# Performance work log

Measured on AMD Instinct MI355X. Metric: run time of the kernel, lower is better.

## Reference

```python
import jax, jax.numpy as jnp
import numpy as np

N = 50000      # nodes
E = 800000     # edges (avg degree 16)
IN_DIM = 128
H = 64         # hidden (GINSmall default)
C = 2          # n_classes
G = 64         # number of graphs in batch


def setup_inputs() -> dict:
    key = jax.random.key(0)
    ks = jax.random.split(key, 16)
    s = 0.05
    inp = {
        "x": jax.random.normal(ks[0], (N, IN_DIM), dtype=jnp.float32),
        "edge_index": jax.random.randint(ks[1], (2, E), 0, N, dtype=jnp.int64),
        "batch": jnp.sort(jax.random.randint(ks[2], (N,), 0, G, dtype=jnp.int64)),
        # conv 0 MLP
        "W1_0": jax.random.normal(ks[3], (IN_DIM, H), dtype=jnp.float32) * s,
        "b1_0": jnp.zeros((H,), jnp.float32),
        "W2_0": jax.random.normal(ks[4], (H, H), dtype=jnp.float32) * s,
        "b2_0": jnp.zeros((H,), jnp.float32),
        # conv 1 MLP
        "W1_1": jax.random.normal(ks[5], (H, H), dtype=jnp.float32) * s,
        "b1_1": jnp.zeros((H,), jnp.float32),
        "W2_1": jax.random.normal(ks[6], (H, H), dtype=jnp.float32) * s,
        "b2_1": jnp.zeros((H,), jnp.float32),
        # conv 2 MLP
        "W1_2": jax.random.normal(ks[7], (H, H), dtype=jnp.float32) * s,
        "b1_2": jnp.zeros((H,), jnp.float32),
        "W2_2": jax.random.normal(ks[8], (H, H), dtype=jnp.float32) * s,
        "b2_2": jnp.zeros((H,), jnp.float32),
        # readout
        "Wl": jax.random.normal(ks[9], (H, C), dtype=jnp.float32) * s,
        "bl": jnp.zeros((C,), jnp.float32),
    }
    return inp


def _gin_conv(h, src, dst, W1, b1, W2, b2):
    # GINConv with eps=0: MLP(h_i + sum_{j->i} h_j)
    agg = jax.ops.segment_sum(h[src], dst, num_segments=N)  # [N, d]
    z = h + agg
    return jnp.maximum(z @ W1 + b1, 0.0) @ W2 + b2


def reference(x, edge_index, batch,
              W1_0, b1_0, W2_0, b2_0,
              W1_1, b1_1, W2_1, b2_1,
              W1_2, b1_2, W2_2, b2_2,
              Wl, bl):
    src, dst = edge_index[0], edge_index[1]  # PyG: messages flow src -> dst
    params = [(W1_0, b1_0, W2_0, b2_0),
              (W1_1, b1_1, W2_1, b2_1),
              (W1_2, b1_2, W2_2, b2_2)]
    h = x
    for (W1, b1, W2, b2) in params:
        h = _gin_conv(h, src, dst, W1, b1, W2, b2)
        h = jnp.maximum(h, 0.0)  # ReLU; dropout is identity at inference
    # global mean pool over graph ids
    sums = jax.ops.segment_sum(h, batch, num_segments=G)          # [G, H]
    cnt = jax.ops.segment_sum(jnp.ones((N,), h.dtype), batch, num_segments=G)
    g = sums / jnp.maximum(cnt, 1.0)[:, None]
    out = g @ Wl + bl
    return out, g
```

## Files before the change

kernel.cpp:

```cpp
#include <hip/hip_runtime.h>

typedef unsigned short ushort_t;
typedef __attribute__((ext_vector_type(8))) short short8;
typedef __attribute__((ext_vector_type(4))) float f32x4;

__device__ inline float bflo(unsigned int u) { return __uint_as_float(u << 16); }
__device__ inline float bfhi(unsigned int u) { return __uint_as_float(u & 0xFFFF0000u); }
__device__ inline unsigned short f2bf(float f) {
    unsigned int u = __float_as_uint(f);
    return (unsigned short)((u + 0x7FFFu + ((u >> 16) & 1u)) >> 16);
}
__device__ inline unsigned int pk(float a, float b) {
    return (unsigned int)f2bf(a) | ((unsigned int)f2bf(b) << 16);
}

union U16B { uint4 u; short8 s; };

__global__ __launch_bounds__(256) void hist_rank(const int* __restrict__ dst,
                                                 int* __restrict__ deg,
                                                 int* __restrict__ rank, int E) {
    int e = blockIdx.x * 256 + threadIdx.x;
    if (e < E) rank[e] = atomicAdd(&deg[dst[e]], 1);
}

__global__ __launch_bounds__(256) void scan_reduce(const int* __restrict__ deg,
                                                   int* __restrict__ bsum, int n) {
    __shared__ int sdata[256];
    int base = blockIdx.x * 1024 + threadIdx.x * 4;
    int s = 0;
#pragma unroll
    for (int k = 0; k < 4; k++) { int i = base + k; if (i < n) s += deg[i]; }
    sdata[threadIdx.x] = s;
    __syncthreads();
    for (int off = 128; off > 0; off >>= 1) {
        if (threadIdx.x < off) sdata[threadIdx.x] += sdata[threadIdx.x + off];
        __syncthreads();
    }
    if (threadIdx.x == 0) bsum[blockIdx.x] = sdata[0];
}

__global__ void scan_bsum(int* __restrict__ bsum, int nb, int* __restrict__ rowptr, int n) {
    if (threadIdx.x == 0 && blockIdx.x == 0) {
        int acc = 0;
        for (int i = 0; i < nb; i++) { int v = bsum[i]; bsum[i] = acc; acc += v; }
        rowptr[n] = acc;
    }
}

__global__ __launch_bounds__(256) void scan_final(const int* __restrict__ deg,
                                                  const int* __restrict__ bsum,
                                                  int* __restrict__ rowptr, int n) {
    __shared__ int sdata[256];
    int t = threadIdx.x;
    int base = blockIdx.x * 1024 + t * 4;
    int v[4]; int s = 0;
#pragma unroll
    for (int k = 0; k < 4; k++) { int i = base + k; v[k] = (i < n) ? deg[i] : 0; s += v[k]; }
    sdata[t] = s;
    __syncthreads();
    for (int off = 1; off < 256; off <<= 1) {
        int x = 0;
        if (t >= off) x = sdata[t - off];
        __syncthreads();
        if (t >= off) sdata[t] += x;
        __syncthreads();
    }
    int off = bsum[blockIdx.x] + sdata[t] - s;
#pragma unroll
    for (int k = 0; k < 4; k++) {
        int i = base + k;
        if (i < n) { rowptr[i] = off; off += v[k]; }
    }
}

__global__ __launch_bounds__(256) void fill_range(const int* __restrict__ src,
                                                  const int* __restrict__ dst,
                                                  const int* __restrict__ rank,
                                                  const int* __restrict__ rowptr,
                                                  int* __restrict__ col, int E, int CE) {
    int range = blockIdx.x & 7;
    int sub = blockIdx.x >> 3;
    int e0 = sub * CE;
    int e1 = min(e0 + CE, E);
    for (int e = e0 + threadIdx.x; e < e1; e += 256) {
        int d = dst[e];
        if ((d >> 13) == range) col[rowptr[d] + rank[e]] = src[e];
    }
}

__global__ __launch_bounds__(256) void gemm_y_mfma(const float* __restrict__ x,
                                                   const float* __restrict__ W1,
                                                   ushort_t* __restrict__ Y, int n) {
    __shared__ ushort_t w1f[4][4][64][8];
    __shared__ ushort_t ybuf[64][72];
    for (int i = threadIdx.x; i < 8192; i += 256) {
        int j = i & 7, lane = (i >> 3) & 63, ct = (i >> 9) & 3, ks = (i >> 11) & 3;
        int k = ks * 32 + ((lane >> 4) << 3) + j;
        int c = ct * 16 + (lane & 15);
        w1f[ks][ct][lane][j] = f2bf(W1[k * 64 + c]);
    }
    __syncthreads();
    int w = threadIdx.x >> 6, lane = threadIdx.x & 63;
    int row0 = blockIdx.x * 64;
    int arow = row0 + w * 16 + (lane & 15);
    if (arow >= n) arow = n - 1;
    const float* xr = x + (size_t)arow * 128;
    int k0base = (lane >> 4) << 3;

    f32x4 acc[4] = {{0,0,0,0},{0,0,0,0},{0,0,0,0},{0,0,0,0}};
#pragma unroll
    for (int ks = 0; ks < 4; ks++) {
        int k0 = ks * 32 + k0base;
        float4 aa = *(const float4*)(xr + k0);
        float4 ab = *(const float4*)(xr + k0 + 4);
        U16B af;
        af.u.x = pk(aa.x, aa.y);
        af.u.y = pk(aa.z, aa.w);
        af.u.z = pk(ab.x, ab.y);
        af.u.w = pk(ab.z, ab.w);
#pragma unroll
        for (int ct = 0; ct < 4; ct++) {
            short8 bf = *(const short8*)&w1f[ks][ct][lane][0];
            acc[ct] = __builtin_amdgcn_mfma_f32_16x16x32_bf16(af.s, bf, acc[ct], 0, 0, 0);
        }
    }
#pragma unroll
    for (int ct = 0; ct < 4; ct++)
#pragma unroll
        for (int r = 0; r < 4; r++)
            ybuf[w * 16 + ((lane >> 4) << 2) + r][ct * 16 + (lane & 15)] = f2bf(acc[ct][r]);
    __syncthreads();
    int row = threadIdx.x >> 2, seg = threadIdx.x & 3;
    if (row0 + row < n) {
        const uint4* p = (const uint4*)&ybuf[row][seg * 16];
        uint4 v0 = p[0], v1 = p[1];
        uint4* q = (uint4*)(Y + (size_t)(row0 + row) * 64 + seg * 16);
        q[0] = v0; q[1] = v1;
    }
}

template <int HASNEXT>
__global__ __launch_bounds__(256) void gfuse(const ushort_t* __restrict__ Y,
                                             const int* __restrict__ rowptr,
                                             const int* __restrict__ col,
                                             const float* __restrict__ b1,
                                             const float* __restrict__ W2,
                                             const float* __restrict__ b2,
                                             const float* __restrict__ Wn,
                                             ushort_t* __restrict__ Yn,
                                             const int* __restrict__ batch,
                                             float* __restrict__ sums, int n) {
    __shared__ ushort_t w2f[2][4][64][8];
    __shared__ ushort_t wnf[HASNEXT ? 2 : 1][4][64][8];
    __shared__ ushort_t st[64][72];
    __shared__ float vbuf[HASNEXT ? 1 : 64][65];
    __shared__ float b1s[64], b2s[64];
    for (int i = threadIdx.x; i < 4096; i += 256) {
        int j = i & 7, lane = (i >> 3) & 63, ct = (i >> 9) & 3, ks = (i >> 11) & 1;
        int k = ks * 32 + ((lane >> 4) << 3) + j;
        int c = ct * 16 + (lane & 15);
        w2f[ks][ct][lane][j] = f2bf(W2[k * 64 + c]);
        if (HASNEXT) wnf[ks][ct][lane][j] = f2bf(Wn[k * 64 + c]);
    }
    if (threadIdx.x < 64) { b1s[threadIdx.x] = b1[threadIdx.x]; b2s[threadIdx.x] = b2[threadIdx.x]; }
    __syncthreads();

    int row0 = blockIdx.x * 64;

    {
        int lr = threadIdx.x >> 2;
        int q  = threadIdx.x & 3;
        int gnode = row0 + lr;
        uint4 o0, o1;
        if (gnode < n) {
            const ushort_t* yb = Y + (size_t)gnode * 64 + q * 16;
            uint4 v0 = *(const uint4*)yb;
            uint4 v1 = *(const uint4*)(yb + 8);
            float ga[16];
            ga[0]=bflo(v0.x); ga[1]=bfhi(v0.x); ga[2]=bflo(v0.y); ga[3]=bfhi(v0.y);
            ga[4]=bflo(v0.z); ga[5]=bfhi(v0.z); ga[6]=bflo(v0.w); ga[7]=bfhi(v0.w);
            ga[8]=bflo(v1.x); ga[9]=bfhi(v1.x); ga[10]=bflo(v1.y); ga[11]=bfhi(v1.y);
            ga[12]=bflo(v1.z); ga[13]=bfhi(v1.z); ga[14]=bflo(v1.w); ga[15]=bfhi(v1.w);
            int e = rowptr[gnode], e1 = rowptr[gnode + 1];
            while (e + 1 < e1) {
                const ushort_t* p0 = Y + (size_t)col[e] * 64 + q * 16;
                const ushort_t* p1 = Y + (size_t)col[e + 1] * 64 + q * 16;
                uint4 a0 = *(const uint4*)p0, a1 = *(const uint4*)(p0 + 8);
                uint4 c0 = *(const uint4*)p1, c1 = *(const uint4*)(p1 + 8);
                ga[0]+=bflo(a0.x)+bflo(c0.x); ga[1]+=bfhi(a0.x)+bfhi(c0.x);
                ga[2]+=bflo(a0.y)+bflo(c0.y); ga[3]+=bfhi(a0.y)+bfhi(c0.y);
                ga[4]+=bflo(a0.z)+bflo(c0.z); ga[5]+=bfhi(a0.z)+bfhi(c0.z);
                ga[6]+=bflo(a0.w)+bflo(c0.w); ga[7]+=bfhi(a0.w)+bfhi(c0.w);
                ga[8]+=bflo(a1.x)+bflo(c1.x); ga[9]+=bfhi(a1.x)+bfhi(c1.x);
                ga[10]+=bflo(a1.y)+bflo(c1.y); ga[11]+=bfhi(a1.y)+bfhi(c1.y);
                ga[12]+=bflo(a1.z)+bflo(c1.z); ga[13]+=bfhi(a1.z)+bfhi(c1.z);
                ga[14]+=bflo(a1.w)+bflo(c1.w); ga[15]+=bfhi(a1.w)+bfhi(c1.w);
                e += 2;
            }
            if (e < e1) {
                const ushort_t* p0 = Y + (size_t)col[e] * 64 + q * 16;
                uint4 a0 = *(const uint4*)p0, a1 = *(const uint4*)(p0 + 8);
                ga[0]+=bflo(a0.x); ga[1]+=bfhi(a0.x); ga[2]+=bflo(a0.y); ga[3]+=bfhi(a0.y);
                ga[4]+=bflo(a0.z); ga[5]+=bfhi(a0.z); ga[6]+=bflo(a0.w); ga[7]+=bfhi(a0.w);
                ga[8]+=bflo(a1.x); ga[9]+=bfhi(a1.x); ga[10]+=bflo(a1.y); ga[11]+=bfhi(a1.y);
                ga[12]+=bflo(a1.z); ga[13]+=bfhi(a1.z); ga[14]+=bflo(a1.w); ga[15]+=bfhi(a1.w);
            }
            int d0 = q * 16;
#pragma unroll
            for (int j = 0; j < 16; j++) ga[j] = fmaxf(ga[j] + b1s[d0 + j], 0.0f);
            o0.x = pk(ga[0], ga[1]);  o0.y = pk(ga[2], ga[3]);
            o0.z = pk(ga[4], ga[5]);  o0.w = pk(ga[6], ga[7]);
            o1.x = pk(ga[8], ga[9]);  o1.y = pk(ga[10], ga[11]);
            o1.z = pk(ga[12], ga[13]); o1.w = pk(ga[14], ga[15]);
        } else {
            o0 = make_uint4(0, 0, 0, 0); o1 = o0;
        }
        *(uint4*)&st[lr][q * 16] = o0;
        *(uint4*)&st[lr][q * 16 + 8] = o1;
    }
    __syncthreads();

    int w = threadIdx.x >> 6, lane = threadIdx.x & 63;
    int k0base = (lane >> 4) << 3;
    f32x4 acc[4] = {{0,0,0,0},{0,0,0,0},{0,0,0,0},{0,0,0,0}};
#pragma unroll
    for (int ks = 0; ks < 2; ks++) {
        short8 af = *(const short8*)&st[w * 16 + (lane & 15)][ks * 32 + k0base];
#pragma unroll
        for (int ct = 0; ct < 4; ct++) {
            short8 bf = *(const short8*)&w2f[ks][ct][lane][0];
            acc[ct] = __builtin_amdgcn_mfma_f32_16x16x32_bf16(af, bf, acc[ct], 0, 0, 0);
        }
    }
    __syncthreads();

    int colb = lane & 15;
    if (HASNEXT) {
#pragma unroll
        for (int ct = 0; ct < 4; ct++)
#pragma unroll
            for (int r = 0; r < 4; r++) {
                float v = fmaxf(acc[ct][r] + b2s[ct * 16 + colb], 0.0f);
                st[w * 16 + ((lane >> 4) << 2) + r][ct * 16 + colb] = f2bf(v);
            }
        __syncthreads();
        f32x4 acc2[4] = {{0,0,0,0},{0,0,0,0},{0,0,0,0},{0,0,0,0}};
#pragma unroll
        for (int ks = 0; ks < 2; ks++) {
            short8 af2 = *(const short8*)&st[w * 16 + (lane & 15)][ks * 32 + k0base];
#pragma unroll
            for (int ct = 0; ct < 4; ct++) {
                short8 bf = *(const short8*)&wnf[ks][ct][lane][0];
                acc2[ct] = __builtin_amdgcn_mfma_f32_16x16x32_bf16(af2, bf, acc2[ct], 0, 0, 0);
            }
        }
        __syncthreads();
#pragma unroll
        for (int ct = 0; ct < 4; ct++)
#pragma unroll
            for (int r = 0; r < 4; r++)
                st[w * 16 + ((lane >> 4) << 2) + r][ct * 16 + colb] = f2bf(acc2[ct][r]);
        __syncthreads();
        int row = threadIdx.x >> 2, seg = threadIdx.x & 3;
        if (row0 + row < n) {
            const uint4* p = (const uint4*)&st[row][seg * 16];
            uint4 v0 = p[0], v1 = p[1];
            uint4* qp = (uint4*)(Yn + (size_t)(row0 + row) * 64 + seg * 16);
            qp[0] = v0; qp[1] = v1;
        }
    } else {
#pragma unroll
        for (int ct = 0; ct < 4; ct++)
#pragma unroll
            for (int r = 0; r < 4; r++) {
                float v = fmaxf(acc[ct][r] + b2s[ct * 16 + colb], 0.0f);
                vbuf[w * 16 + ((lane >> 4) << 2) + r][ct * 16 + colb] = v;
            }
        __syncthreads();
        int j  = threadIdx.x & 63;
        int i0 = (threadIdx.x >> 6) * 16;
        int cur = -1; float a = 0.0f;
        for (int i = i0; i < i0 + 16; i++) {
            int row = row0 + i;
            if (row >= n) break;
            int b = batch[row];
            if (b != cur) {
                if (cur >= 0) atomicAdd(&sums[cur * 64 + j], a);
                cur = b; a = 0.0f;
            }
            a += vbuf[i][j];
        }
        if (cur >= 0) atomicAdd(&sums[cur * 64 + j], a);
    }
}

__global__ __launch_bounds__(64) void finalize_kernel(const float* __restrict__ sums,
                                                      const int* __restrict__ batch, int n,
                                                      const float* __restrict__ Wl,
                                                      const float* __restrict__ bl,
                                                      float* __restrict__ out, int G) {
    int g = blockIdx.x;
    int j = threadIdx.x;
    __shared__ float gs[64];
    int lo = 0, hi = n;
    while (lo < hi) { int m = (lo + hi) >> 1; if (batch[m] < g) lo = m + 1; else hi = m; }
    int lo2 = lo, hi2 = n;
    while (lo2 < hi2) { int m = (lo2 + hi2) >> 1; if (batch[m] < g + 1) lo2 = m + 1; else hi2 = m; }
    float c = (float)max(lo2 - lo, 1);
    float v = sums[g * 64 + j] / c;
    gs[j] = v;
    out[G * 2 + g * 64 + j] = v;
    __syncthreads();
    if (j < 2) {
        float acc = bl[j];
#pragma unroll
        for (int k = 0; k < 64; k++) acc += gs[k] * Wl[k * 2 + j];
        out[g * 2 + j] = acc;
    }
}

extern "C" void kernel_launch(void* const* d_in, const int* in_sizes, int n_in,
                              void* d_out, int out_size, void* d_ws, size_t ws_size,
                              hipStream_t stream) {
    const float* x     = (const float*)d_in[0];
    const int*   ei    = (const int*)d_in[1];
    const int*   batch = (const int*)d_in[2];
    const float* W1_0 = (const float*)d_in[3];
    const float* b1_0 = (const float*)d_in[4];
    const float* W2_0 = (const float*)d_in[5];
    const float* b2_0 = (const float*)d_in[6];
    const float* W1_1 = (const float*)d_in[7];
    const float* b1_1 = (const float*)d_in[8];
    const float* W2_1 = (const float*)d_in[9];
    const float* b2_1 = (const float*)d_in[10];
    const float* W1_2 = (const float*)d_in[11];
    const float* b1_2 = (const float*)d_in[12];
    const float* W2_2 = (const float*)d_in[13];
    const float* b2_2 = (const float*)d_in[14];
    const float* Wl   = (const float*)d_in[15];
    const float* bl   = (const float*)d_in[16];

    const int N = in_sizes[0] / 128;
    const int E = in_sizes[1] / 2;
    const int G = out_size / 66;
    const int* src = ei;
    const int* dst = ei + E;
    float* out = (float*)d_out;

    const int nb = (N + 1023) / 1024;

    ushort_t* Y   = (ushort_t*)d_ws;
    ushort_t* Y2  = Y + (size_t)N * 64;
    float* sums   = (float*)(Y2 + (size_t)N * 64);
    int*   deg    = (int*)(sums + (size_t)G * 64);
    int*   rowptr = deg + N;
    int*   col    = rowptr + (N + 1);
    int*   rank   = col + E;
    int*   bsum   = rank + E;

    hipMemsetAsync(sums, 0, ((size_t)G * 64 + N) * sizeof(int), stream);

    hist_rank<<<(E + 255) / 256, 256, 0, stream>>>(dst, deg, rank, E);
    scan_reduce<<<nb, 256, 0, stream>>>(deg, bsum, N);
    scan_bsum<<<1, 64, 0, stream>>>(bsum, nb, rowptr, N);
    scan_final<<<nb, 256, 0, stream>>>(deg, bsum, rowptr, N);
    const int SUBS = 64;
    const int CE = (E + SUBS - 1) / SUBS;
    fill_range<<<8 * SUBS, 256, 0, stream>>>(src, dst, rank, rowptr, col, E, CE);

    const int mblk = (N + 63) / 64;

    gemm_y_mfma<<<mblk, 256, 0, stream>>>(x, W1_0, Y, N);
    gfuse<1><<<mblk, 256, 0, stream>>>(Y, rowptr, col, b1_0, W2_0, b2_0, W1_1, Y2, nullptr, nullptr, N);
    gfuse<1><<<mblk, 256, 0, stream>>>(Y2, rowptr, col, b1_1, W2_1, b2_1, W1_2, Y, nullptr, nullptr, N);
    gfuse<0><<<mblk, 256, 0, stream>>>(Y, rowptr, col, b1_2, W2_2, b2_2, nullptr, nullptr, batch, sums, N);
    finalize_kernel<<<G, 64, 0, stream>>>(sums, batch, N, Wl, bl, out, G);
}
```

Before: 186.8 us.

## Fuse CSR construction into a single cooperative kernel with grid syncs

The memset plus the histogram/rank, three-stage scan and fill kernels are replaced by one cooperative kernel of 256 blocks. Grid-wide syncs separate zeroing, histogram, block scan, partial scan, rowptr write and column fill. The intent is to remove several launch gaps and the serial single-thread bucket scan. In exchange it adds grid-sync cost, uses fewer blocks for the fill phase, and depends on cooperative launch support and on N being at most 65536 for the one-element-per-thread scan.

Result: slower. 341.7 us (+83.0%).

```diff
diff --git a/kernel.cpp b/kernel.cpp
--- a/kernel.cpp
+++ b/kernel.cpp
@@ -1,4 +1,7 @@
 #include <hip/hip_runtime.h>
+#include <hip/hip_cooperative_groups.h>
+
+namespace cg = cooperative_groups;
 
 typedef unsigned short ushort_t;
 typedef __attribute__((ext_vector_type(8))) short short8;
@@ -16,75 +19,71 @@
 
 union U16B { uint4 u; short8 s; };
 
-__global__ __launch_bounds__(256) void hist_rank(const int* __restrict__ dst,
-                                                 int* __restrict__ deg,
-                                                 int* __restrict__ rank, int E) {
-    int e = blockIdx.x * 256 + threadIdx.x;
-    if (e < E) rank[e] = atomicAdd(&deg[dst[e]], 1);
-}
-
-__global__ __launch_bounds__(256) void scan_reduce(const int* __restrict__ deg,
-                                                   int* __restrict__ bsum, int n) {
+__global__ __launch_bounds__(256) void csr_coop(const int* __restrict__ dst,
+                                                const int* __restrict__ src,
+                                                int* __restrict__ deg,
+                                                int* __restrict__ rank,
+                                                int* __restrict__ rowptr,
+                                                int* __restrict__ col,
+                                                int* __restrict__ partials,
+                                                int* __restrict__ bpre,
+                                                float* __restrict__ sums,
+                                                int E, int N, int SZ, int CE) {
+    cg::grid_group grid = cg::this_grid();
     __shared__ int sdata[256];
-    int base = blockIdx.x * 1024 + threadIdx.x * 4;
-    int s = 0;
-#pragma unroll
-    for (int k = 0; k < 4; k++) { int i = base + k; if (i < n) s += deg[i]; }
-    sdata[threadIdx.x] = s;
-    __syncthreads();
-    for (int off = 128; off > 0; off >>= 1) {
-        if (threadIdx.x < off) sdata[threadIdx.x] += sdata[threadIdx.x + off];
-        __syncthreads();
-    }
-    if (threadIdx.x == 0) bsum[blockIdx.x] = sdata[0];
-}
-
-__global__ void scan_bsum(int* __restrict__ bsum, int nb, int* __restrict__ rowptr, int n) {
-    if (threadIdx.x == 0 && blockIdx.x == 0) {
-        int acc = 0;
-        for (int i = 0; i < nb; i++) { int v = bsum[i]; bsum[i] = acc; acc += v; }
-        rowptr[n] = acc;
-    }
-}
-
-__global__ __launch_bounds__(256) void scan_final(const int* __restrict__ deg,
-                                                  const int* __restrict__ bsum,
-                                                  int* __restrict__ rowptr, int n) {
-    __shared__ int sdata[256];
-    int t = threadIdx.x;
-    int base = blockIdx.x * 1024 + t * 4;
-    int v[4]; int s = 0;
-#pragma unroll
-    for (int k = 0; k < 4; k++) { int i = base + k; v[k] = (i < n) ? deg[i] : 0; s += v[k]; }
-    sdata[t] = s;
+    const int tid = threadIdx.x;
+    const int gsize = gridDim.x * 256;
+    const int gtid = blockIdx.x * 256 + tid;
+
+    for (int i = gtid; i < N; i += gsize) deg[i] = 0;
+    for (int i = gtid; i < SZ; i += gsize) sums[i] = 0.0f;
+    grid.sync();
+
+    for (int e = gtid; e < E; e += gsize) rank[e] = atomicAdd(&deg[dst[e]], 1);
+    grid.sync();
+
+    int v = (gtid < N) ? deg[gtid] : 0;
+    sdata[tid] = v;
     __syncthreads();
     for (int off = 1; off < 256; off <<= 1) {
         int x = 0;
-        if (t >= off) x = sdata[t - off];
-        __syncthreads();
-        if (t >= off) sdata[t] += x;
-        __syncthreads();
-    }
-    int off = bsum[blockIdx.x] + sdata[t] - s;
-#pragma unroll
-    for (int k = 0; k < 4; k++) {
-        int i = base + k;
-        if (i < n) { rowptr[i] = off; off += v[k]; }
-    }
-}
-
-__global__ __launch_bounds__(256) void fill_range(const int* __restrict__ src,
-                                                  const int* __restrict__ dst,
-                                                  const int* __restrict__ rank,
-                                                  const int* __restrict__ rowptr,
-                                                  int* __restrict__ col, int E, int CE) {
-    int range = blockIdx.x & 7;
-    int sub = blockIdx.x >> 3;
-    int e0 = sub * CE;
-    int e1 = min(e0 + CE, E);
-    for (int e = e0 + threadIdx.x; e < e1; e += 256) {
-        int d = dst[e];
-        if ((d >> 13) == range) col[rowptr[d] + rank[e]] = src[e];
+        if (tid >= off) x = sdata[tid - off];
+        __syncthreads();
+        if (tid >= off) sdata[tid] += x;
+        __syncthreads();
+    }
+    int ex = sdata[tid] - v;
+    if (tid == 255) partials[blockIdx.x] = sdata[255];
+    grid.sync();
+
+    if (blockIdx.x == 0) {
+        int p = partials[tid];
+        sdata[tid] = p;
+        __syncthreads();
+        for (int off = 1; off < 256; off <<= 1) {
+            int x = 0;
+            if (tid >= off) x = sdata[tid - off];
+            __syncthreads();
+            if (tid >= off) sdata[tid] += x;
+            __syncthreads();
+        }
+        bpre[tid] = sdata[tid] - p;
+        if (tid == 255) rowptr[N] = sdata[255];
+    }
+    grid.sync();
+
+    if (gtid < N) rowptr[gtid] = bpre[blockIdx.x] + ex;
+    grid.sync();
+
+    {
+        int range = blockIdx.x & 7;
+        int sub = blockIdx.x >> 3;
+        int e0 = sub * CE;
+        int e1 = min(e0 + CE, E);
+        for (int e = e0 + tid; e < e1; e += 256) {
+            int d = dst[e];
+            if ((d >> 13) == range) col[rowptr[d] + rank[e]] = src[e];
+        }
     }
 }
 
@@ -347,8 +346,6 @@
     const int* dst = ei + E;
     float* out = (float*)d_out;
 
-    const int nb = (N + 1023) / 1024;
-
     ushort_t* Y   = (ushort_t*)d_ws;
     ushort_t* Y2  = Y + (size_t)N * 64;
     float* sums   = (float*)(Y2 + (size_t)N * 64);
@@ -356,17 +353,18 @@
     int*   rowptr = deg + N;
     int*   col    = rowptr + (N + 1);
     int*   rank   = col + E;
-    int*   bsum   = rank + E;
-
-    hipMemsetAsync(sums, 0, ((size_t)G * 64 + N) * sizeof(int), stream);
-
-    hist_rank<<<(E + 255) / 256, 256, 0, stream>>>(dst, deg, rank, E);
-    scan_reduce<<<nb, 256, 0, stream>>>(deg, bsum, N);
-    scan_bsum<<<1, 64, 0, stream>>>(bsum, nb, rowptr, N);
-    scan_final<<<nb, 256, 0, stream>>>(deg, bsum, rowptr, N);
-    const int SUBS = 64;
-    const int CE = (E + SUBS - 1) / SUBS;
-    fill_range<<<8 * SUBS, 256, 0, stream>>>(src, dst, rank, rowptr, col, E, CE);
+    int*   partials = rank + E;
+    int*   bpre   = partials + 256;
+
+    const int SZ = G * 64;
+    const int CE = (E + 31) / 32;
+
+    {
+        void* args[] = {(void*)&dst, (void*)&src, (void*)&deg, (void*)&rank,
+                        (void*)&rowptr, (void*)&col, (void*)&partials, (void*)&bpre,
+                        (void*)&sums, (void*)&E, (void*)&N, (void*)&SZ, (void*)&CE};
+        hipLaunchCooperativeKernel((void*)csr_coop, dim3(256), dim3(256), args, 0, stream);
+    }
 
     const int mblk = (N + 63) / 64;
 
```

## Merge histogram with first GEMM and collapse three-kernel scan into one

Applied to the files above, without the earlier changes.

The degree histogram/rank pass now runs as extra blocks inside the first-layer MFMA GEMM launch, so the two independent jobs share one launch and can overlap. The three scan kernels are replaced by a single 64-block kernel that publishes per-block totals through flags and spin-waits on them for a decoupled prefix. This removes several launches and serial gaps. The spin-wait assumes all 64 blocks are co-resident and that N fits in 64×1024 entries, which is hardcoded.

Result: faster. 173.9 us (-6.9%).

```diff
diff --git a/kernel.cpp b/kernel.cpp
--- a/kernel.cpp
+++ b/kernel.cpp
@@ -16,43 +16,76 @@
 
 union U16B { uint4 u; short8 s; };
 
-__global__ __launch_bounds__(256) void hist_rank(const int* __restrict__ dst,
+#define HB 512
+
+__global__ __launch_bounds__(256) void gemm_hist(const float* __restrict__ x,
+                                                 const float* __restrict__ W1,
+                                                 ushort_t* __restrict__ Y, int n,
+                                                 const int* __restrict__ dst,
                                                  int* __restrict__ deg,
                                                  int* __restrict__ rank, int E) {
-    int e = blockIdx.x * 256 + threadIdx.x;
-    if (e < E) rank[e] = atomicAdd(&deg[dst[e]], 1);
-}
-
-__global__ __launch_bounds__(256) void scan_reduce(const int* __restrict__ deg,
-                                                   int* __restrict__ bsum, int n) {
+    if (blockIdx.x < HB) {
+        for (int e = blockIdx.x * 256 + threadIdx.x; e < E; e += HB * 256)
+            rank[e] = atomicAdd(&deg[dst[e]], 1);
+        return;
+    }
+    __shared__ ushort_t w1f[4][4][64][8];
+    __shared__ ushort_t ybuf[64][72];
+    for (int i = threadIdx.x; i < 8192; i += 256) {
+        int j = i & 7, lane = (i >> 3) & 63, ct = (i >> 9) & 3, ks = (i >> 11) & 3;
+        int k = ks * 32 + ((lane >> 4) << 3) + j;
+        int c = ct * 16 + (lane & 15);
+        w1f[ks][ct][lane][j] = f2bf(W1[k * 64 + c]);
+    }
+    __syncthreads();
+    int w = threadIdx.x >> 6, lane = threadIdx.x & 63;
+    int row0 = (blockIdx.x - HB) * 64;
+    int arow = row0 + w * 16 + (lane & 15);
+    if (arow >= n) arow = n - 1;
+    const float* xr = x + (size_t)arow * 128;
+    int k0base = (lane >> 4) << 3;
+
+    f32x4 acc[4] = {{0,0,0,0},{0,0,0,0},{0,0,0,0},{0,0,0,0}};
+#pragma unroll
+    for (int ks = 0; ks < 4; ks++) {
+        int k0 = ks * 32 + k0base;
+        float4 aa = *(const float4*)(xr + k0);
+        float4 ab = *(const float4*)(xr + k0 + 4);
+        U16B af;
+        af.u.x = pk(aa.x, aa.y);
+        af.u.y = pk(aa.z, aa.w);
+        af.u.z = pk(ab.x, ab.y);
+        af.u.w = pk(ab.z, ab.w);
+#pragma unroll
+        for (int ct = 0; ct < 4; ct++) {
+            short8 bf = *(const short8*)&w1f[ks][ct][lane][0];
+            acc[ct] = __builtin_amdgcn_mfma_f32_16x16x32_bf16(af.s, bf, acc[ct], 0, 0, 0);
+        }
+    }
+#pragma unroll
+    for (int ct = 0; ct < 4; ct++)
+#pragma unroll
+        for (int r = 0; r < 4; r++)
+            ybuf[w * 16 + ((lane >> 4) << 2) + r][ct * 16 + (lane & 15)] = f2bf(acc[ct][r]);
+    __syncthreads();
+    int row = threadIdx.x >> 2, seg = threadIdx.x & 3;
+    if (row0 + row < n) {
+        const uint4* p = (const uint4*)&ybuf[row][seg * 16];
+        uint4 v0 = p[0], v1 = p[1];
+        uint4* q = (uint4*)(Y + (size_t)(row0 + row) * 64 + seg * 16);
+        q[0] = v0; q[1] = v1;
+    }
+}
+
+__global__ __launch_bounds__(256) void scan_all(const int* __restrict__ deg,
+                                                int* __restrict__ rowptr,
+                                                int* __restrict__ aggr,
+                                                int* __restrict__ flags, int n) {
     __shared__ int sdata[256];
-    int base = blockIdx.x * 1024 + threadIdx.x * 4;
-    int s = 0;
-#pragma unroll
-    for (int k = 0; k < 4; k++) { int i = base + k; if (i < n) s += deg[i]; }
-    sdata[threadIdx.x] = s;
-    __syncthreads();
-    for (int off = 128; off > 0; off >>= 1) {
-        if (threadIdx.x < off) sdata[threadIdx.x] += sdata[threadIdx.x + off];
-        __syncthreads();
-    }
-    if (threadIdx.x == 0) bsum[blockIdx.x] = sdata[0];
-}
-
-__global__ void scan_bsum(int* __restrict__ bsum, int nb, int* __restrict__ rowptr, int n) {
-    if (threadIdx.x == 0 && blockIdx.x == 0) {
-        int acc = 0;
-        for (int i = 0; i < nb; i++) { int v = bsum[i]; bsum[i] = acc; acc += v; }
-        rowptr[n] = acc;
-    }
-}
-
-__global__ __launch_bounds__(256) void scan_final(const int* __restrict__ deg,
-                                                  const int* __restrict__ bsum,
-                                                  int* __restrict__ rowptr, int n) {
-    __shared__ int sdata[256];
+    __shared__ int sagg[64];
+    int b = blockIdx.x;
     int t = threadIdx.x;
-    int base = blockIdx.x * 1024 + t * 4;
+    int base = b * 1024 + t * 4;
     int v[4]; int s = 0;
 #pragma unroll
     for (int k = 0; k < 4; k++) { int i = base + k; v[k] = (i < n) ? deg[i] : 0; s += v[k]; }
@@ -65,12 +98,25 @@
         if (t >= off) sdata[t] += x;
         __syncthreads();
     }
-    int off = bsum[blockIdx.x] + sdata[t] - s;
+    int ex = sdata[t] - s;
+    if (t == 255) {
+        aggr[b] = sdata[255];
+        __threadfence();
+        atomicExch(&flags[b], 1);
+    }
+    if (t < 64) { while (atomicAdd(&flags[t], 0) == 0) {} }
+    __syncthreads();
+    if (t < 64) sagg[t] = aggr[t];
+    __syncthreads();
+    int bp = 0;
+    for (int i = 0; i < b; i++) bp += sagg[i];
+    int off = bp + ex;
 #pragma unroll
     for (int k = 0; k < 4; k++) {
         int i = base + k;
         if (i < n) { rowptr[i] = off; off += v[k]; }
     }
+    if (b == 63 && t == 255) rowptr[n] = bp + sdata[255];
 }
 
 __global__ __launch_bounds__(256) void fill_range(const int* __restrict__ src,
@@ -85,57 +131,6 @@
     for (int e = e0 + threadIdx.x; e < e1; e += 256) {
         int d = dst[e];
         if ((d >> 13) == range) col[rowptr[d] + rank[e]] = src[e];
-    }
-}
-
-__global__ __launch_bounds__(256) void gemm_y_mfma(const float* __restrict__ x,
-                                                   const float* __restrict__ W1,
-                                                   ushort_t* __restrict__ Y, int n) {
-    __shared__ ushort_t w1f[4][4][64][8];
-    __shared__ ushort_t ybuf[64][72];
-    for (int i = threadIdx.x; i < 8192; i += 256) {
-        int j = i & 7, lane = (i >> 3) & 63, ct = (i >> 9) & 3, ks = (i >> 11) & 3;
-        int k = ks * 32 + ((lane >> 4) << 3) + j;
-        int c = ct * 16 + (lane & 15);
-        w1f[ks][ct][lane][j] = f2bf(W1[k * 64 + c]);
-    }
-    __syncthreads();
-    int w = threadIdx.x >> 6, lane = threadIdx.x & 63;
-    int row0 = blockIdx.x * 64;
-    int arow = row0 + w * 16 + (lane & 15);
-    if (arow >= n) arow = n - 1;
-    const float* xr = x + (size_t)arow * 128;
-    int k0base = (lane >> 4) << 3;
-
-    f32x4 acc[4] = {{0,0,0,0},{0,0,0,0},{0,0,0,0},{0,0,0,0}};
-#pragma unroll
-    for (int ks = 0; ks < 4; ks++) {
-        int k0 = ks * 32 + k0base;
-        float4 aa = *(const float4*)(xr + k0);
-        float4 ab = *(const float4*)(xr + k0 + 4);
-        U16B af;
-        af.u.x = pk(aa.x, aa.y);
-        af.u.y = pk(aa.z, aa.w);
-        af.u.z = pk(ab.x, ab.y);
-        af.u.w = pk(ab.z, ab.w);
-#pragma unroll
-        for (int ct = 0; ct < 4; ct++) {
-            short8 bf = *(const short8*)&w1f[ks][ct][lane][0];
-            acc[ct] = __builtin_amdgcn_mfma_f32_16x16x32_bf16(af.s, bf, acc[ct], 0, 0, 0);
-        }
-    }
-#pragma unroll
-    for (int ct = 0; ct < 4; ct++)
-#pragma unroll
-        for (int r = 0; r < 4; r++)
-            ybuf[w * 16 + ((lane >> 4) << 2) + r][ct * 16 + (lane & 15)] = f2bf(acc[ct][r]);
-    __syncthreads();
-    int row = threadIdx.x >> 2, seg = threadIdx.x & 3;
-    if (row0 + row < n) {
-        const uint4* p = (const uint4*)&ybuf[row][seg * 16];
-        uint4 v0 = p[0], v1 = p[1];
-        uint4* q = (uint4*)(Y + (size_t)(row0 + row) * 64 + seg * 16);
-        q[0] = v0; q[1] = v1;
     }
 }
 
@@ -347,30 +342,26 @@
     const int* dst = ei + E;
     float* out = (float*)d_out;
 
-    const int nb = (N + 1023) / 1024;
-
     ushort_t* Y   = (ushort_t*)d_ws;
     ushort_t* Y2  = Y + (size_t)N * 64;
     float* sums   = (float*)(Y2 + (size_t)N * 64);
     int*   deg    = (int*)(sums + (size_t)G * 64);
-    int*   rowptr = deg + N;
+    int*   flags  = deg + N;
+    int*   rowptr = flags + 64;
     int*   col    = rowptr + (N + 1);
     int*   rank   = col + E;
-    int*   bsum   = rank + E;
-
-    hipMemsetAsync(sums, 0, ((size_t)G * 64 + N) * sizeof(int), stream);
-
-    hist_rank<<<(E + 255) / 256, 256, 0, stream>>>(dst, deg, rank, E);
-    scan_reduce<<<nb, 256, 0, stream>>>(deg, bsum, N);
-    scan_bsum<<<1, 64, 0, stream>>>(bsum, nb, rowptr, N);
-    scan_final<<<nb, 256, 0, stream>>>(deg, bsum, rowptr, N);
+    int*   aggr   = rank + E;
+
+    hipMemsetAsync(sums, 0, ((size_t)G * 64 + N + 64) * sizeof(int), stream);
+
+    const int mblk = (N + 63) / 64;
+
+    gemm_hist<<<HB + mblk, 256, 0, stream>>>(x, W1_0, Y, N, dst, deg, rank, E);
+    scan_all<<<64, 256, 0, stream>>>(deg, rowptr, aggr, flags, N);
     const int SUBS = 64;
     const int CE = (E + SUBS - 1) / SUBS;
     fill_range<<<8 * SUBS, 256, 0, stream>>>(src, dst, rank, rowptr, col, E, CE);
 
-    const int mblk = (N + 63) / 64;
-
-    gemm_y_mfma<<<mblk, 256, 0, stream>>>(x, W1_0, Y, N);
     gfuse<1><<<mblk, 256, 0, stream>>>(Y, rowptr, col, b1_0, W2_0, b2_0, W1_1, Y2, nullptr, nullptr, N);
     gfuse<1><<<mblk, 256, 0, stream>>>(Y2, rowptr, col, b1_1, W2_1, b2_1, W1_2, Y, nullptr, nullptr, N);
     gfuse<0><<<mblk, 256, 0, stream>>>(Y, rowptr, col, b1_2, W2_2, b2_2, nullptr, nullptr, batch, sums, N);
```
